# Optimization experiments

Measured on AMD Instinct MI355X. Metric: run time of the kernel, lower is better.

The kernel has to match this reference:

```python
import jax, jax.numpy as jnp
import numpy as np

EPS = 1e-5

def _layernorm(h):
    mu = jnp.mean(h, axis=-1, keepdims=True)
    var = jnp.mean(jnp.square(h - mu), axis=-1, keepdims=True)
    return (h - mu) / jnp.sqrt(var + EPS)

def _mlp_silu_ln(h, w_in, b_in, w_out, b_out):
    h = jax.nn.relu(h @ w_in + b_in) @ w_out + b_out
    h = h * jax.nn.sigmoid(h)  # SiLU as written: x * sigmoid(x)
    return _layernorm(h)

def setup_inputs() -> dict:
    key = jax.random.key(0)
    N, E, D_IN, D, L = 50000, 800000, 16, 64, 4
    ks = jax.random.split(key, 12)
    s = lambda *sh: 1.0 / np.sqrt(sh[0])
    return {
        "x": jax.random.normal(ks[0], (N, D_IN), dtype=jnp.float32),
        "edge_index": jax.random.randint(ks[1], (2, E), 0, N, dtype=jnp.int32),
        "w0": jax.random.normal(ks[2], (D_IN, D), dtype=jnp.float32) * s(D_IN),
        "b0": jnp.zeros((D,), dtype=jnp.float32),
        "w1": jax.random.normal(ks[3], (D, D), dtype=jnp.float32) * s(D),
        "b1": jnp.zeros((D,), dtype=jnp.float32),
        "wa": jax.random.normal(ks[4], (L, D, 2 * D), dtype=jnp.float32) * s(D),
        "ba": jnp.zeros((L, 2 * D), dtype=jnp.float32),
        "wb": jax.random.normal(ks[5], (L, 2 * D, D), dtype=jnp.float32) * s(2 * D),
        "bb": jnp.zeros((L, D), dtype=jnp.float32),
    }

def reference(x, edge_index, w0, b0, w1, b1, wa, ba, wb, bb):
    N = x.shape[0]
    src, dst = edge_index[0], edge_index[1]  # PyG: row=source j, col=target i
    # InitialEmbedding
    h = _mlp_silu_ln(x, w0, b0, w1, b1)
    ones = jnp.ones((src.shape[0],), dtype=h.dtype)
    cnt = jax.ops.segment_sum(ones, dst, num_segments=N)
    denom = jnp.maximum(cnt, 1.0)[:, None]  # mean aggr; 0 for isolated nodes
    for l in range(wa.shape[0]):
        m = _mlp_silu_ln(h, wa[l], ba[l], wb[l], bb[l])
        agg = jax.ops.segment_sum(m[src], dst, num_segments=N) / denom
        h = agg + h  # residual in MeshGNN.forward
    return h
```

## Files before the change

kernel.cpp:

```cpp
#include <hip/hip_runtime.h>
#include <hip/hip_fp16.h>
#include <math.h>

#define D_IN 16
#define D    64
#define H    128
#define EPSL 1e-5f

typedef _Float16 h2v __attribute__((ext_vector_type(2)));

__device__ __forceinline__ float dot2f(unsigned int a, unsigned int b, float c)
{
#if __has_builtin(__builtin_amdgcn_fdot2)
    return __builtin_amdgcn_fdot2(__builtin_bit_cast(h2v, a),
                                  __builtin_bit_cast(h2v, b), c, false);
#else
    __half2 ha = *reinterpret_cast<__half2*>(&a);
    __half2 hb = *reinterpret_cast<__half2*>(&b);
    float2 fa = __half22float2(ha), fb = __half22float2(hb);
    return fmaf(fa.x, fb.x, fmaf(fa.y, fb.y, c));
#endif
}

__device__ __forceinline__ unsigned int packh2(float x, float y)
{
    __half2 p = __floats2half2_rn(x, y);
    return *reinterpret_cast<unsigned int*>(&p);
}


__global__ void k_zero2(int* __restrict__ a, int* __restrict__ b, int n)
{
    int i = blockIdx.x * blockDim.x + threadIdx.x;
    if (i < n) { a[i] = 0; b[i] = 0; }
}

__global__ void k_hist(const int* __restrict__ dst, int* __restrict__ cnt, int E)
{
    int i = blockIdx.x * blockDim.x + threadIdx.x;
    if (i < E) atomicAdd(&cnt[dst[i]], 1);
}

__global__ void k_scan_blk(const int* __restrict__ cnt, int* __restrict__ off,
                           int* __restrict__ bsum, int N)
{
    __shared__ int sm[256];
    int t = threadIdx.x;
    int g = blockIdx.x * 256 + t;
    int v = (g < N) ? cnt[g] : 0;
    sm[t] = v;
    __syncthreads();
    for (int d2 = 1; d2 < 256; d2 <<= 1) {
        int u = (t >= d2) ? sm[t - d2] : 0;
        __syncthreads();
        sm[t] += u;
        __syncthreads();
    }
    if (g < N) off[g + 1] = sm[t];
    if (t == 255) bsum[blockIdx.x] = sm[255];
}

__global__ void k_scan_top(int* __restrict__ bsum, int G)
{
    __shared__ int sm[1024];
    int t = threadIdx.x;
    int v = (t < G) ? bsum[t] : 0;
    sm[t] = v;
    __syncthreads();
    for (int d2 = 1; d2 < 1024; d2 <<= 1) {
        int u = (t >= d2) ? sm[t - d2] : 0;
        __syncthreads();
        sm[t] += u;
        __syncthreads();
    }
    if (t < G) bsum[t] = sm[t] - v;
}

__global__ void k_scan_add(int* __restrict__ off, const int* __restrict__ bsum, int N)
{
    int g = blockIdx.x * 256 + threadIdx.x;
    if (g < N) off[g + 1] += bsum[blockIdx.x];
    if (g == 0) off[0] = 0;
}

__global__ __launch_bounds__(256) void k_fill_x(const int* __restrict__ src,
                                                const int* __restrict__ dst,
                                                const int* __restrict__ off,
                                                int* __restrict__ fill,
                                                int* __restrict__ csr, int E)
{
    int g = blockIdx.x & 7;
    int j = blockIdx.x >> 3;
    int J = gridDim.x >> 3;
    int e0     = (j * 256 + threadIdx.x) * 4;
    int stride = J * 256 * 4;

#define PROC(dv, sv) \
    if (((dv >> 4) & 7) == g) { \
        int o_ = off[dv]; \
        int p_ = atomicAdd(&fill[dv], 1); \
        csr[o_ + p_] = sv; \
    }

    for (int e = e0; e < E; e += stride) {
        if (e + 3 < E) {
            int4 d4 = *(const int4*)(dst + e);
            int4 s4 = *(const int4*)(src + e);
            PROC(d4.x, s4.x)
            PROC(d4.y, s4.y)
            PROC(d4.z, s4.z)
            PROC(d4.w, s4.w)
        } else {
            for (int k = e; k < E; ++k) {
                int dv = dst[k];
                int sv = src[k];
                PROC(dv, sv)
            }
        }
    }
#undef PROC
}

__global__ void k_prep_w(const float* __restrict__ wa, const float* __restrict__ wb,
                         unsigned int* __restrict__ wap, unsigned int* __restrict__ wbp,
                         int L)
{
    int idx = blockIdx.x * blockDim.x + threadIdx.x;
    if (idx >= L * 8192) return;
    int l = idx >> 13;
    int r = idx & 8191;
    if (r < 4096) {
        int k2 = r >> 7, c = r & 127;
        const float* base = wa + (size_t)l * D * H;
        wap[(size_t)l * 4096 + r] = packh2(base[(2 * k2) * H + c],
                                           base[(2 * k2 + 1) * H + c]);
    } else {
        r -= 4096;
        int k2 = r >> 6, j = r & 63;
        const float* base = wb + (size_t)l * H * D;
        wbp[(size_t)l * 4096 + r] = packh2(base[(2 * k2) * D + j],
                                           base[(2 * k2 + 1) * D + j]);
    }
}

__global__ __launch_bounds__(256) void k_mlp(const float* __restrict__ h,
                                             const unsigned int* __restrict__ wap,
                                             const float* __restrict__ ba,
                                             const unsigned int* __restrict__ wbp,
                                             const float* __restrict__ bb,
                                             __half* __restrict__ m, int N)
{
    __shared__ __align__(16) unsigned int hT2[32 * 64];
    __shared__ __align__(16) unsigned int gT2[64 * 64];

    const int tid  = threadIdx.x;
    const int ch   = tid & 15;
    const int q    = tid >> 4;
    const int base = blockIdx.x * 64;

    {
        int sn = tid & 63;
        int sc = tid >> 6;
        int gn = min(base + sn, N - 1);
        const float4* hp = (const float4*)(h + (size_t)gn * D + sc * 16);
        float4 A = hp[0], B = hp[1], C = hp[2], Dv = hp[3];
        unsigned int* w = hT2 + (sc * 8) * 64 + sn;
        w[0 * 64] = packh2(A.x, A.y);  w[1 * 64] = packh2(A.z, A.w);
        w[2 * 64] = packh2(B.x, B.y);  w[3 * 64] = packh2(B.z, B.w);
        w[4 * 64] = packh2(C.x, C.y);  w[5 * 64] = packh2(C.z, C.w);
        w[6 * 64] = packh2(Dv.x, Dv.y); w[7 * 64] = packh2(Dv.z, Dv.w);
    }
    __syncthreads();

    float acc[4][8];
#pragma unroll
    for (int i = 0; i < 4; ++i)
#pragma unroll
        for (int c = 0; c < 8; ++c) acc[i][c] = 0.f;

#pragma unroll 4
    for (int k2 = 0; k2 < 32; ++k2) {
        const unsigned int* wr = wap + k2 * 128 + ch * 8;
        uint4 w0 = *(const uint4*)(wr);
        uint4 w1 = *(const uint4*)(wr + 4);
        uint4 hh = *(const uint4*)(hT2 + k2 * 64 + q * 4);
#define P1(i, hv) \
        acc[i][0]=dot2f(hv,w0.x,acc[i][0]); acc[i][1]=dot2f(hv,w0.y,acc[i][1]); \
        acc[i][2]=dot2f(hv,w0.z,acc[i][2]); acc[i][3]=dot2f(hv,w0.w,acc[i][3]); \
        acc[i][4]=dot2f(hv,w1.x,acc[i][4]); acc[i][5]=dot2f(hv,w1.y,acc[i][5]); \
        acc[i][6]=dot2f(hv,w1.z,acc[i][6]); acc[i][7]=dot2f(hv,w1.w,acc[i][7]);
        P1(0, hh.x) P1(1, hh.y) P1(2, hh.z) P1(3, hh.w)
#undef P1
    }

    {
        float4 b0v = *(const float4*)(ba + ch * 8);
        float4 b1v = *(const float4*)(ba + ch * 8 + 4);
        float bav[8] = {b0v.x, b0v.y, b0v.z, b0v.w, b1v.x, b1v.y, b1v.z, b1v.w};
#pragma unroll
        for (int cc = 0; cc < 4; ++cc) {
            int c0 = 2 * cc, c1 = 2 * cc + 1;
            int r2 = ch * 4 + cc;
            int chunk = q ^ (r2 & 15);
            uint4 t;
            t.x = packh2(fmaxf(acc[0][c0] + bav[c0], 0.f), fmaxf(acc[0][c1] + bav[c1], 0.f));
            t.y = packh2(fmaxf(acc[1][c0] + bav[c0], 0.f), fmaxf(acc[1][c1] + bav[c1], 0.f));
            t.z = packh2(fmaxf(acc[2][c0] + bav[c0], 0.f), fmaxf(acc[2][c1] + bav[c1], 0.f));
            t.w = packh2(fmaxf(acc[3][c0] + bav[c0], 0.f), fmaxf(acc[3][c1] + bav[c1], 0.f));
            *(uint4*)(gT2 + r2 * 64 + chunk * 4) = t;
        }
    }
    __syncthreads();

    float oo[4][4];
#pragma unroll
    for (int i = 0; i < 4; ++i)
#pragma unroll
        for (int j = 0; j < 4; ++j) oo[i][j] = 0.f;

#pragma unroll 8
    for (int k2 = 0; k2 < 64; ++k2) {
        uint4 w = *(const uint4*)(wbp + k2 * 64 + ch * 4);
        int chunk = q ^ (k2 & 15);
        uint4 g = *(const uint4*)(gT2 + k2 * 64 + chunk * 4);
#define P2(i, gv) \
        oo[i][0]=dot2f(gv,w.x,oo[i][0]); oo[i][1]=dot2f(gv,w.y,oo[i][1]); \
        oo[i][2]=dot2f(gv,w.z,oo[i][2]); oo[i][3]=dot2f(gv,w.w,oo[i][3]);
        P2(0, g.x) P2(1, g.y) P2(2, g.z) P2(3, g.w)
#undef P2
    }

    float4 bbv = *(const float4*)(bb + ch * 4);
    float bz[4] = {bbv.x, bbv.y, bbv.z, bbv.w};
    float s[4], qv[4];
#pragma unroll
    for (int i = 0; i < 4; ++i) {
        float ss = 0.f, qq = 0.f;
#pragma unroll
        for (int j = 0; j < 4; ++j) {
            float t = oo[i][j] + bz[j];
            t = t / (1.f + __expf(-t));
            oo[i][j] = t;
            ss += t;
            qq = fmaf(t, t, qq);
        }
        s[i] = ss; qv[i] = qq;
    }

#pragma unroll
    for (int d2 = 1; d2 < 16; d2 <<= 1) {
#pragma unroll
        for (int i = 0; i < 4; ++i) {
            s[i]  += __shfl_xor(s[i],  d2, 64);
            qv[i] += __shfl_xor(qv[i], d2, 64);
        }
    }

#pragma unroll
    for (int i = 0; i < 4; ++i) {
        float mu  = s[i] * (1.f / D);
        float var = qv[i] * (1.f / D) - mu * mu;
        float inv = rsqrtf(var + EPSL);
        int node = base + q * 4 + i;
        if (node < N) {
            uint2 pk;
            pk.x = packh2((oo[i][0] - mu) * inv, (oo[i][1] - mu) * inv);
            pk.y = packh2((oo[i][2] - mu) * inv, (oo[i][3] - mu) * inv);
            *(uint2*)(m + (size_t)node * D + ch * 4) = pk;
        }
    }
}

__global__ __launch_bounds__(256) void k_init(const float* __restrict__ x,
                                              const float* __restrict__ w0,
                                              const float* __restrict__ b0,
                                              const float* __restrict__ w1,
                                              const float* __restrict__ b1,
                                              float* __restrict__ h, int N)
{
    __shared__ __align__(16) float xT[D_IN * 64];
    __shared__ __align__(16) float gT[D * 64];

    const int tid  = threadIdx.x;
    const int ch   = tid & 15;
    const int q    = tid >> 4;
    const int base = blockIdx.x * 64;

    {
        int sn = tid & 63;
        int sc = tid >> 6;
        int gn = min(base + sn, N - 1);
        float4 xv = *(const float4*)(x + (size_t)gn * D_IN + sc * 4);
        float* w = xT + (sc * 4) * 64 + sn;
        w[0*64] = xv.x; w[1*64] = xv.y; w[2*64] = xv.z; w[3*64] = xv.w;
    }
    __syncthreads();

    float acc[4][4];
#pragma unroll
    for (int i = 0; i < 4; ++i)
#pragma unroll
        for (int c = 0; c < 4; ++c) acc[i][c] = 0.f;

#pragma unroll
    for (int k = 0; k < D_IN; ++k) {
        float4 w = *(const float4*)(w0 + k * D + ch * 4);
        float4 xv = *(const float4*)(xT + k * 64 + q * 4);
#define PP(i, xc) \
        acc[i][0]=fmaf(xc,w.x,acc[i][0]); acc[i][1]=fmaf(xc,w.y,acc[i][1]); \
        acc[i][2]=fmaf(xc,w.z,acc[i][2]); acc[i][3]=fmaf(xc,w.w,acc[i][3]);
        PP(0, xv.x) PP(1, xv.y) PP(2, xv.z) PP(3, xv.w)
#undef PP
    }

    {
        float4 b0v = *(const float4*)(b0 + ch * 4);
        float bav[4] = {b0v.x, b0v.y, b0v.z, b0v.w};
        int chunk = q ^ (ch >> 1);
#pragma unroll
        for (int c = 0; c < 4; ++c) {
            int r = ch * 4 + c;
            float4 t;
            t.x = fmaxf(acc[0][c] + bav[c], 0.f);
            t.y = fmaxf(acc[1][c] + bav[c], 0.f);
            t.z = fmaxf(acc[2][c] + bav[c], 0.f);
            t.w = fmaxf(acc[3][c] + bav[c], 0.f);
            *(float4*)(gT + r * 64 + chunk * 4) = t;
        }
    }
    __syncthreads();

    float4 o0 = {0,0,0,0}, o1 = {0,0,0,0}, o2 = {0,0,0,0}, o3 = {0,0,0,0};
#pragma unroll 8
    for (int k = 0; k < D; ++k) {
        float4 w = *(const float4*)(w1 + k * D + ch * 4);
        int chunk = q ^ ((k >> 3) & 15);
        float4 g = *(const float4*)(gT + k * 64 + chunk * 4);
        o0.x=fmaf(g.x,w.x,o0.x); o0.y=fmaf(g.x,w.y,o0.y); o0.z=fmaf(g.x,w.z,o0.z); o0.w=fmaf(g.x,w.w,o0.w);
        o1.x=fmaf(g.y,w.x,o1.x); o1.y=fmaf(g.y,w.y,o1.y); o1.z=fmaf(g.y,w.z,o1.z); o1.w=fmaf(g.y,w.w,o1.w);
        o2.x=fmaf(g.z,w.x,o2.x); o2.y=fmaf(g.z,w.y,o2.y); o2.z=fmaf(g.z,w.z,o2.z); o2.w=fmaf(g.z,w.w,o2.w);
        o3.x=fmaf(g.w,w.x,o3.x); o3.y=fmaf(g.w,w.y,o3.y); o3.z=fmaf(g.w,w.z,o3.z); o3.w=fmaf(g.w,w.w,o3.w);
    }

    float4 bbv = *(const float4*)(b1 + ch * 4);
    float s[4], qv[4];
#define FIN(i, ov) { \
        ov.x += bbv.x; ov.y += bbv.y; ov.z += bbv.z; ov.w += bbv.w; \
        ov.x = ov.x / (1.f + __expf(-ov.x)); ov.y = ov.y / (1.f + __expf(-ov.y)); \
        ov.z = ov.z / (1.f + __expf(-ov.z)); ov.w = ov.w / (1.f + __expf(-ov.w)); \
        s[i]  = (ov.x + ov.y) + (ov.z + ov.w); \
        qv[i] = fmaf(ov.x, ov.x, fmaf(ov.y, ov.y, fmaf(ov.z, ov.z, ov.w * ov.w))); }
    FIN(0, o0) FIN(1, o1) FIN(2, o2) FIN(3, o3)
#undef FIN

#pragma unroll
    for (int d2 = 1; d2 < 16; d2 <<= 1) {
#pragma unroll
        for (int i = 0; i < 4; ++i) {
            s[i]  += __shfl_xor(s[i],  d2, 64);
            qv[i] += __shfl_xor(qv[i], d2, 64);
        }
    }

#pragma unroll
    for (int i = 0; i < 4; ++i) {
        float mu  = s[i] * (1.f / D);
        float var = qv[i] * (1.f / D) - mu * mu;
        float inv = rsqrtf(var + EPSL);
        int node = base + q * 4 + i;
        if (node < N) {
            float4 ov = (i == 0) ? o0 : (i == 1) ? o1 : (i == 2) ? o2 : o3;
            float4 outv;
            outv.x = (ov.x - mu) * inv;
            outv.y = (ov.y - mu) * inv;
            outv.z = (ov.z - mu) * inv;
            outv.w = (ov.w - mu) * inv;
            *(float4*)(h + (size_t)node * D + ch * 4) = outv;
        }
    }
}

__global__ __launch_bounds__(256) void k_agg(const __half* __restrict__ m,
                                             const int* __restrict__ csr,
                                             const int* __restrict__ off,
                                             float* __restrict__ h, int N)
{
    int g = threadIdx.x >> 4;
    int c = threadIdx.x & 15;
    int node = blockIdx.x * 16 + g;
    if (node >= N) return;

    int b  = off[node];
    int e2 = off[node + 1];
    float4 s0 = {0.f, 0.f, 0.f, 0.f};
    float4 s1 = {0.f, 0.f, 0.f, 0.f};
    int e = b;
#define GATH(sacc, pv) { \
        float2 u0 = __half22float2(*reinterpret_cast<__half2*>(&pv.x)); \
        float2 u1 = __half22float2(*reinterpret_cast<__half2*>(&pv.y)); \
        sacc.x += u0.x; sacc.y += u0.y; sacc.z += u1.x; sacc.w += u1.y; }
    for (; e + 4 <= e2; e += 4) {
        int sn0 = csr[e], sn1 = csr[e + 1], sn2 = csr[e + 2], sn3 = csr[e + 3];
        int2 p0 = ((const int2*)(m + (size_t)sn0 * D))[c];
        int2 p1 = ((const int2*)(m + (size_t)sn1 * D))[c];
        int2 p2 = ((const int2*)(m + (size_t)sn2 * D))[c];
        int2 p3 = ((const int2*)(m + (size_t)sn3 * D))[c];
        GATH(s0, p0) GATH(s1, p1) GATH(s0, p2) GATH(s1, p3)
    }
    for (; e < e2; ++e) {
        int sn = csr[e];
        int2 p = ((const int2*)(m + (size_t)sn * D))[c];
        GATH(s0, p)
    }
#undef GATH
    s0.x += s1.x; s0.y += s1.y; s0.z += s1.z; s0.w += s1.w;

    float dnm = fmaxf((float)(e2 - b), 1.f);
    float inv = 1.f / dnm;

    float4* hp = (float4*)(h + (size_t)node * D);
    float4 hv = hp[c];
    hv.x = fmaf(s0.x, inv, hv.x);
    hv.y = fmaf(s0.y, inv, hv.y);
    hv.z = fmaf(s0.z, inv, hv.z);
    hv.w = fmaf(s0.w, inv, hv.w);
    hp[c] = hv;
}

extern "C" void kernel_launch(void* const* d_in, const int* in_sizes, int n_in,
                              void* d_out, int out_size, void* d_ws, size_t ws_size,
                              hipStream_t stream)
{
    const float* x  = (const float*)d_in[0];
    const int*   ei = (const int*)d_in[1];
    const float* w0 = (const float*)d_in[2];
    const float* b0 = (const float*)d_in[3];
    const float* w1 = (const float*)d_in[4];
    const float* b1 = (const float*)d_in[5];
    const float* wa = (const float*)d_in[6];
    const float* ba = (const float*)d_in[7];
    const float* wb = (const float*)d_in[8];
    const float* bb = (const float*)d_in[9];

    const int N = in_sizes[0] / D_IN;
    const int E = in_sizes[1] / 2;
    const int L = in_sizes[6] / (D * H);

    const int* src = ei;
    const int* dst = ei + E;

    char* ws = (char*)d_ws;
    size_t o = 0;
    auto carve = [&](size_t bytes) -> char* {
        char* p = ws + o;
        o = (o + bytes + 255) & ~(size_t)255;
        return p;
    };
    __half* m          = (__half*)carve((size_t)N * D * sizeof(__half));
    int*   csr         = (int*)  carve((size_t)E * sizeof(int));
    int*   cnt         = (int*)  carve((size_t)N * sizeof(int));
    int*   fill        = (int*)  carve((size_t)N * sizeof(int));
    int*   offp        = (int*)  carve((size_t)(N + 1) * sizeof(int));
    int*   bsum        = (int*)  carve((size_t)1024 * sizeof(int));
    unsigned int* wap  = (unsigned int*)carve((size_t)L * 4096 * sizeof(unsigned int));
    unsigned int* wbp  = (unsigned int*)carve((size_t)L * 4096 * sizeof(unsigned int));

    float* h = (float*)d_out;

    const int nb = (N + 63) / 64;
    const int G1 = (N + 255) / 256;

    k_zero2<<<(N + 255) / 256, 256, 0, stream>>>(cnt, fill, N);
    k_hist<<<(E + 255) / 256, 256, 0, stream>>>(dst, cnt, E);
    k_scan_blk<<<G1, 256, 0, stream>>>(cnt, offp, bsum, N);
    k_scan_top<<<1, 1024, 0, stream>>>(bsum, G1);
    k_scan_add<<<G1, 256, 0, stream>>>(offp, bsum, N);
    k_fill_x<<<2048, 256, 0, stream>>>(src, dst, offp, fill, csr, E);
    k_prep_w<<<(L * 8192 + 255) / 256, 256, 0, stream>>>(wa, wb, wap, wbp, L);

    k_init<<<nb, 256, 0, stream>>>(x, w0, b0, w1, b1, h, N);

    for (int l = 0; l < L; ++l) {
        k_mlp<<<nb, 256, 0, stream>>>(h, wap + (size_t)l * 4096,
                                      ba + (size_t)l * H,
                                      wbp + (size_t)l * 4096,
                                      bb + (size_t)l * D, m, N);
        k_agg<<<(N + 15) / 16, 256, 0, stream>>>(m, csr, offp, h, N);
    }
}
```

Baseline: 303.4 us.

## Use MFMA 16x16x32 f16 matrix cores for the per-layer MLP

```diff
diff --git a/kernel.cpp b/kernel.cpp
--- a/kernel.cpp
+++ b/kernel.cpp
@@ -7,20 +7,11 @@
 #define H    128
 #define EPSL 1e-5f
 
-typedef _Float16 h2v __attribute__((ext_vector_type(2)));
-
-__device__ __forceinline__ float dot2f(unsigned int a, unsigned int b, float c)
-{
-#if __has_builtin(__builtin_amdgcn_fdot2)
-    return __builtin_amdgcn_fdot2(__builtin_bit_cast(h2v, a),
-                                  __builtin_bit_cast(h2v, b), c, false);
-#else
-    __half2 ha = *reinterpret_cast<__half2*>(&a);
-    __half2 hb = *reinterpret_cast<__half2*>(&b);
-    float2 fa = __half22float2(ha), fb = __half22float2(hb);
-    return fmaf(fa.x, fb.x, fmaf(fa.y, fb.y, c));
-#endif
-}
+typedef _Float16 h2v  __attribute__((ext_vector_type(2)));
+typedef _Float16 f16x8 __attribute__((ext_vector_type(8)));
+typedef float    f32x4v __attribute__((ext_vector_type(4)));
+
+union FU { uint4 u; f16x8 h; };
 
 __device__ __forceinline__ unsigned int packh2(float x, float y)
 {
@@ -122,151 +113,154 @@
 }
 
 __global__ void k_prep_w(const float* __restrict__ wa, const float* __restrict__ wb,
-                         unsigned int* __restrict__ wap, unsigned int* __restrict__ wbp,
+                         unsigned int* __restrict__ waf, unsigned int* __restrict__ wbf,
                          int L)
 {
     int idx = blockIdx.x * blockDim.x + threadIdx.x;
     if (idx >= L * 8192) return;
     int l = idx >> 13;
     int r = idx & 8191;
-    if (r < 4096) {
-        int k2 = r >> 7, c = r & 127;
-        const float* base = wa + (size_t)l * D * H;
-        wap[(size_t)l * 4096 + r] = packh2(base[(2 * k2) * H + c],
-                                           base[(2 * k2 + 1) * H + c]);
+    bool isA = (r < 4096);
+    int r2   = isA ? r : r - 4096;
+    int u    = r2 & 3;
+    int lane = (r2 >> 2) & 63;
+    int t    = r2 >> 8;
+    int g  = lane >> 4;
+    int li = lane & 15;
+    int kk = (u < 2) ? (4 * g + 2 * u) : (16 + 4 * g + 2 * (u - 2));
+    if (isA) {
+        int kb = t & 1, ct = t >> 1;
+        int c  = ct * 16 + li;
+        int k0 = kb * 32 + kk;
+        const float* bse = wa + (size_t)l * D * H;
+        waf[(size_t)l * 4096 + r2] = packh2(bse[k0 * H + c], bse[(k0 + 1) * H + c]);
     } else {
-        r -= 4096;
-        int k2 = r >> 6, j = r & 63;
-        const float* base = wb + (size_t)l * H * D;
-        wbp[(size_t)l * 4096 + r] = packh2(base[(2 * k2) * D + j],
-                                           base[(2 * k2 + 1) * D + j]);
+        int kb = t & 3, c2 = t >> 2;
+        int j  = c2 * 16 + li;
+        int k0 = kb * 32 + kk;
+        const float* bse = wb + (size_t)l * H * D;
+        wbf[(size_t)l * 4096 + r2] = packh2(bse[k0 * D + j], bse[(k0 + 1) * D + j]);
     }
 }
 
 __global__ __launch_bounds__(256) void k_mlp(const float* __restrict__ h,
-                                             const unsigned int* __restrict__ wap,
+                                             const unsigned int* __restrict__ waf,
                                              const float* __restrict__ ba,
-                                             const unsigned int* __restrict__ wbp,
+                                             const unsigned int* __restrict__ wbf,
                                              const float* __restrict__ bb,
                                              __half* __restrict__ m, int N)
 {
-    __shared__ __align__(16) unsigned int hT2[32 * 64];
-    __shared__ __align__(16) unsigned int gT2[64 * 64];
+    __shared__ __align__(16) unsigned int hpk[64 * 38];
+    __shared__ __align__(16) float        Pf[64 * 132];
 
     const int tid  = threadIdx.x;
-    const int ch   = tid & 15;
-    const int q    = tid >> 4;
+    const int w    = tid >> 6;
+    const int lane = tid & 63;
+    const int g    = lane >> 4;
+    const int li   = lane & 15;
     const int base = blockIdx.x * 64;
 
     {
-        int sn = tid & 63;
-        int sc = tid >> 6;
+        int sn = tid & 63, sc = tid >> 6;
         int gn = min(base + sn, N - 1);
         const float4* hp = (const float4*)(h + (size_t)gn * D + sc * 16);
         float4 A = hp[0], B = hp[1], C = hp[2], Dv = hp[3];
-        unsigned int* w = hT2 + (sc * 8) * 64 + sn;
-        w[0 * 64] = packh2(A.x, A.y);  w[1 * 64] = packh2(A.z, A.w);
-        w[2 * 64] = packh2(B.x, B.y);  w[3 * 64] = packh2(B.z, B.w);
-        w[4 * 64] = packh2(C.x, C.y);  w[5 * 64] = packh2(C.z, C.w);
-        w[6 * 64] = packh2(Dv.x, Dv.y); w[7 * 64] = packh2(Dv.z, Dv.w);
-    }
-    __syncthreads();
-
-    float acc[4][8];
-#pragma unroll
-    for (int i = 0; i < 4; ++i)
-#pragma unroll
-        for (int c = 0; c < 8; ++c) acc[i][c] = 0.f;
-
-#pragma unroll 4
-    for (int k2 = 0; k2 < 32; ++k2) {
-        const unsigned int* wr = wap + k2 * 128 + ch * 8;
-        uint4 w0 = *(const uint4*)(wr);
-        uint4 w1 = *(const uint4*)(wr + 4);
-        uint4 hh = *(const uint4*)(hT2 + k2 * 64 + q * 4);
-#define P1(i, hv) \
-        acc[i][0]=dot2f(hv,w0.x,acc[i][0]); acc[i][1]=dot2f(hv,w0.y,acc[i][1]); \
-        acc[i][2]=dot2f(hv,w0.z,acc[i][2]); acc[i][3]=dot2f(hv,w0.w,acc[i][3]); \
-        acc[i][4]=dot2f(hv,w1.x,acc[i][4]); acc[i][5]=dot2f(hv,w1.y,acc[i][5]); \
-        acc[i][6]=dot2f(hv,w1.z,acc[i][6]); acc[i][7]=dot2f(hv,w1.w,acc[i][7]);
-        P1(0, hh.x) P1(1, hh.y) P1(2, hh.z) P1(3, hh.w)
-#undef P1
-    }
-
+        unsigned int* wp = hpk + sn * 38 + sc * 8;
+        wp[0] = packh2(A.x, A.y);  wp[1] = packh2(A.z, A.w);
+        wp[2] = packh2(B.x, B.y);  wp[3] = packh2(B.z, B.w);
+        wp[4] = packh2(C.x, C.y);  wp[5] = packh2(C.z, C.w);
+        wp[6] = packh2(Dv.x, Dv.y); wp[7] = packh2(Dv.z, Dv.w);
+    }
+    __syncthreads();
+
+    FU A0, A1;
     {
-        float4 b0v = *(const float4*)(ba + ch * 8);
-        float4 b1v = *(const float4*)(ba + ch * 8 + 4);
-        float bav[8] = {b0v.x, b0v.y, b0v.z, b0v.w, b1v.x, b1v.y, b1v.z, b1v.w};
-#pragma unroll
-        for (int cc = 0; cc < 4; ++cc) {
-            int c0 = 2 * cc, c1 = 2 * cc + 1;
-            int r2 = ch * 4 + cc;
-            int chunk = q ^ (r2 & 15);
-            uint4 t;
-            t.x = packh2(fmaxf(acc[0][c0] + bav[c0], 0.f), fmaxf(acc[0][c1] + bav[c1], 0.f));
-            t.y = packh2(fmaxf(acc[1][c0] + bav[c0], 0.f), fmaxf(acc[1][c1] + bav[c1], 0.f));
-            t.z = packh2(fmaxf(acc[2][c0] + bav[c0], 0.f), fmaxf(acc[2][c1] + bav[c1], 0.f));
-            t.w = packh2(fmaxf(acc[3][c0] + bav[c0], 0.f), fmaxf(acc[3][c1] + bav[c1], 0.f));
-            *(uint4*)(gT2 + r2 * 64 + chunk * 4) = t;
-        }
-    }
-    __syncthreads();
-
-    float oo[4][4];
-#pragma unroll
-    for (int i = 0; i < 4; ++i)
-#pragma unroll
-        for (int j = 0; j < 4; ++j) oo[i][j] = 0.f;
-
-#pragma unroll 8
-    for (int k2 = 0; k2 < 64; ++k2) {
-        uint4 w = *(const uint4*)(wbp + k2 * 64 + ch * 4);
-        int chunk = q ^ (k2 & 15);
-        uint4 g = *(const uint4*)(gT2 + k2 * 64 + chunk * 4);
-#define P2(i, gv) \
-        oo[i][0]=dot2f(gv,w.x,oo[i][0]); oo[i][1]=dot2f(gv,w.y,oo[i][1]); \
-        oo[i][2]=dot2f(gv,w.z,oo[i][2]); oo[i][3]=dot2f(gv,w.w,oo[i][3]);
-        P2(0, g.x) P2(1, g.y) P2(2, g.z) P2(3, g.w)
-#undef P2
-    }
-
-    float4 bbv = *(const float4*)(bb + ch * 4);
-    float bz[4] = {bbv.x, bbv.y, bbv.z, bbv.w};
-    float s[4], qv[4];
-#pragma unroll
-    for (int i = 0; i < 4; ++i) {
-        float ss = 0.f, qq = 0.f;
-#pragma unroll
-        for (int j = 0; j < 4; ++j) {
-            float t = oo[i][j] + bz[j];
+        const unsigned int* ap = hpk + (16 * w + li) * 38;
+        uint2 x0 = *(const uint2*)(ap + 2 * g);
+        uint2 x1 = *(const uint2*)(ap + 8 + 2 * g);
+        uint2 x2 = *(const uint2*)(ap + 16 + 2 * g);
+        uint2 x3 = *(const uint2*)(ap + 24 + 2 * g);
+        A0.u = make_uint4(x0.x, x0.y, x1.x, x1.y);
+        A1.u = make_uint4(x2.x, x2.y, x3.x, x3.y);
+    }
+
+    f32x4v acc[8];
+#pragma unroll
+    for (int ct = 0; ct < 8; ++ct) {
+        FU b0, b1;
+        b0.u = ((const uint4*)waf)[(ct * 2 + 0) * 64 + lane];
+        b1.u = ((const uint4*)waf)[(ct * 2 + 1) * 64 + lane];
+        f32x4v a = {0.f, 0.f, 0.f, 0.f};
+        a = __builtin_amdgcn_mfma_f32_16x16x32_f16(A0.h, b0.h, a, 0, 0, 0);
+        a = __builtin_amdgcn_mfma_f32_16x16x32_f16(A1.h, b1.h, a, 0, 0, 0);
+        acc[ct] = a;
+    }
+
+#pragma unroll
+    for (int ct = 0; ct < 8; ++ct) {
+        float bav = ba[ct * 16 + li];
+#pragma unroll
+        for (int r = 0; r < 4; ++r) {
+            int node = 16 * w + 4 * g + r;
+            Pf[node * 132 + ct * 16 + li] = fmaxf(acc[ct][r] + bav, 0.f);
+        }
+    }
+    __syncthreads();
+
+    f32x4v acc2[4];
+#pragma unroll
+    for (int c2 = 0; c2 < 4; ++c2) acc2[c2] = (f32x4v){0.f, 0.f, 0.f, 0.f};
+
+    const float* pp = Pf + (16 * w + li) * 132;
+#pragma unroll
+    for (int kb = 0; kb < 4; ++kb) {
+        float4 plo = *(const float4*)(pp + 32 * kb + 4 * g);
+        float4 phi = *(const float4*)(pp + 32 * kb + 16 + 4 * g);
+        FU Af;
+        Af.u = make_uint4(packh2(plo.x, plo.y), packh2(plo.z, plo.w),
+                          packh2(phi.x, phi.y), packh2(phi.z, phi.w));
+#pragma unroll
+        for (int c2 = 0; c2 < 4; ++c2) {
+            FU b;
+            b.u = ((const uint4*)wbf)[(c2 * 4 + kb) * 64 + lane];
+            acc2[c2] = __builtin_amdgcn_mfma_f32_16x16x32_f16(Af.h, b.h, acc2[c2], 0, 0, 0);
+        }
+    }
+
+    float sv[4] = {0.f, 0.f, 0.f, 0.f};
+    float qv[4] = {0.f, 0.f, 0.f, 0.f};
+#pragma unroll
+    for (int c2 = 0; c2 < 4; ++c2) {
+        float bbv = bb[c2 * 16 + li];
+#pragma unroll
+        for (int r = 0; r < 4; ++r) {
+            float t = acc2[c2][r] + bbv;
             t = t / (1.f + __expf(-t));
-            oo[i][j] = t;
-            ss += t;
-            qq = fmaf(t, t, qq);
-        }
-        s[i] = ss; qv[i] = qq;
-    }
-
+            acc2[c2][r] = t;
+            sv[r] += t;
+            qv[r] = fmaf(t, t, qv[r]);
+        }
+    }
 #pragma unroll
     for (int d2 = 1; d2 < 16; d2 <<= 1) {
 #pragma unroll
-        for (int i = 0; i < 4; ++i) {
-            s[i]  += __shfl_xor(s[i],  d2, 64);
-            qv[i] += __shfl_xor(qv[i], d2, 64);
-        }
-    }
-
-#pragma unroll
-    for (int i = 0; i < 4; ++i) {
-        float mu  = s[i] * (1.f / D);
-        float var = qv[i] * (1.f / D) - mu * mu;
-        float inv = rsqrtf(var + EPSL);
-        int node = base + q * 4 + i;
+        for (int r = 0; r < 4; ++r) {
+            sv[r] += __shfl_xor(sv[r], d2, 64);
+            qv[r] += __shfl_xor(qv[r], d2, 64);
+        }
+    }
+#pragma unroll
+    for (int r = 0; r < 4; ++r) {
+        int node = base + 16 * w + 4 * g + r;
         if (node < N) {
-            uint2 pk;
-            pk.x = packh2((oo[i][0] - mu) * inv, (oo[i][1] - mu) * inv);
-            pk.y = packh2((oo[i][2] - mu) * inv, (oo[i][3] - mu) * inv);
-            *(uint2*)(m + (size_t)node * D + ch * 4) = pk;
+            float mu  = sv[r] * (1.f / D);
+            float var = qv[r] * (1.f / D) - mu * mu;
+            float inv = rsqrtf(var + EPSL);
+#pragma unroll
+            for (int c2 = 0; c2 < 4; ++c2) {
+                m[(size_t)node * D + c2 * 16 + li] =
+                    __float2half((acc2[c2][r] - mu) * inv);
+            }
         }
     }
 }
@@ -462,8 +456,8 @@
     int*   fill        = (int*)  carve((size_t)N * sizeof(int));
     int*   offp        = (int*)  carve((size_t)(N + 1) * sizeof(int));
     int*   bsum        = (int*)  carve((size_t)1024 * sizeof(int));
-    unsigned int* wap  = (unsigned int*)carve((size_t)L * 4096 * sizeof(unsigned int));
-    unsigned int* wbp  = (unsigned int*)carve((size_t)L * 4096 * sizeof(unsigned int));
+    unsigned int* waf  = (unsigned int*)carve((size_t)L * 4096 * sizeof(unsigned int));
+    unsigned int* wbf  = (unsigned int*)carve((size_t)L * 4096 * sizeof(unsigned int));
 
     float* h = (float*)d_out;
 
@@ -476,14 +470,14 @@
     k_scan_top<<<1, 1024, 0, stream>>>(bsum, G1);
     k_scan_add<<<G1, 256, 0, stream>>>(offp, bsum, N);
     k_fill_x<<<2048, 256, 0, stream>>>(src, dst, offp, fill, csr, E);
-    k_prep_w<<<(L * 8192 + 255) / 256, 256, 0, stream>>>(wa, wb, wap, wbp, L);
+    k_prep_w<<<(L * 8192 + 255) / 256, 256, 0, stream>>>(wa, wb, waf, wbf, L);
 
     k_init<<<nb, 256, 0, stream>>>(x, w0, b0, w1, b1, h, N);
 
     for (int l = 0; l < L; ++l) {
-        k_mlp<<<nb, 256, 0, stream>>>(h, wap + (size_t)l * 4096,
+        k_mlp<<<nb, 256, 0, stream>>>(h, waf + (size_t)l * 4096,
                                       ba + (size_t)l * H,
-                                      wbp + (size_t)l * 4096,
+                                      wbf + (size_t)l * 4096,
                                       bb + (size_t)l * D, m, N);
         k_agg<<<(N + 15) / 16, 256, 0, stream>>>(m, csr, offp, h, N);
     }
```

After: 250.4 us. 17.5% less time.
